# Kernel tuning notes

Measured on AMD Instinct MI355X. Metric: run time of the kernel, lower is better.

Reference implementation:

```python
import jax, jax.numpy as jnp
import numpy as np

B, L, D, H, DK, DV = 512, 256, 1024, 16, 64, 64
TEMP = float(np.sqrt(D))  # source uses sqrt(d_model), not sqrt(d_k)
LN_EPS = 1.0              # LayerNormalization default eps=1, added to std


def setup_inputs() -> dict:
    key = jax.random.key(0)
    ks = jax.random.split(key, 7)
    u = lambda k, shape: jax.random.uniform(k, shape, jnp.float32, -0.04, 0.04)
    return {
        "q": jax.random.normal(ks[0], (B, D), jnp.float32),
        "k": jax.random.normal(ks[1], (B, L, D), jnp.float32),
        "v": jax.random.normal(ks[2], (B, L, D), jnp.float32),
        "Wq": u(ks[3], (H, DK, D)),   # stacked per-head q-proj weights
        "Wk": u(ks[4], (H, DK, D)),
        "Wv": u(ks[5], (H, DV, D)),
        "Wp": u(ks[6], (D, H * DV)),  # output projection (nn.Linear weight layout)
        "scale": jnp.ones((D,), jnp.float32),
        "offset": jnp.zeros((D,), jnp.float32),
    }


def reference(q, k, v, Wq, Wk, Wv, Wp, scale, offset):
    # per-head projections (batched over heads instead of a Python loop)
    hq = jnp.einsum('bd,hkd->bhk', q, Wq)       # [B,H,DK]
    hk = jnp.einsum('bld,hkd->bhlk', k, Wk)     # [B,H,L,DK]
    hv = jnp.einsum('bld,hvd->bhlv', v, Wv)     # [B,H,L,DV]
    # single-query dot-product attention per head
    scores = jnp.einsum('bhk,bhlk->bhl', hq, hk) / TEMP
    w = jax.nn.softmax(scores, axis=-1)         # dropout is identity (rate 0 / eval)
    ctx = jnp.einsum('bhl,bhlv->bhv', w, hv).reshape(B, H * DV)
    # output projection + residual
    out = ctx @ Wp.T + q
    # LayerNormalization: unbiased std (torch.std default), eps added to std
    mean = out.mean(axis=-1, keepdims=True)
    std = jnp.sqrt(jnp.sum((out - mean) ** 2, axis=-1, keepdims=True) / (D - 1))
    return scale * (out - mean) / (std + LN_EPS) + offset
```

## Files before the change

### kernel.cpp

```cpp
#include <hip/hip_runtime.h>

#define B_ 512
#define L_ 256
#define D_ 1024
#define H_ 16
#define DK_ 64
#define DV_ 64

typedef float f32x4 __attribute__((ext_vector_type(4)));
typedef float f32x2 __attribute__((ext_vector_type(2)));
typedef __bf16 bf16x8 __attribute__((ext_vector_type(8)));
typedef __bf16 bf16x2 __attribute__((ext_vector_type(2)));

#define MFMA16(a, b, c) __builtin_amdgcn_mfma_f32_16x16x32_bf16((a), (b), (c), 0, 0, 0)

__device__ inline bf16x8 cvt8(f32x4 a, f32x4 b) {
  bf16x8 r;
  r[0] = (__bf16)a[0]; r[1] = (__bf16)a[1]; r[2] = (__bf16)a[2]; r[3] = (__bf16)a[3];
  r[4] = (__bf16)b[0]; r[5] = (__bf16)b[1]; r[6] = (__bf16)b[2]; r[7] = (__bf16)b[3];
  return r;
}

__global__ __launch_bounds__(256) void k_hq(const float* __restrict__ q,
                                            const float* __restrict__ Wq,
                                            __bf16* __restrict__ hq) {
  int tid = threadIdx.x, lane = tid & 63, wid = tid >> 6;
  int r16 = lane & 15, g = lane >> 4;
  int n0 = (blockIdx.x * 4 + wid) * 16;
  int m0 = blockIdx.y * 16;
  const float* arow = q  + (size_t)(m0 + r16) * D_;
  const float* brow = Wq + (size_t)(n0 + r16) * D_;
  f32x4 acc = {0.f, 0.f, 0.f, 0.f};
  for (int ks = 0; ks < D_ / 32; ++ks) {
    int k0 = ks * 32 + g * 8;
    f32x4 a0 = *(const f32x4*)(arow + k0);
    f32x4 a1 = *(const f32x4*)(arow + k0 + 4);
    f32x4 b0 = *(const f32x4*)(brow + k0);
    f32x4 b1 = *(const f32x4*)(brow + k0 + 4);
    acc = MFMA16(cvt8(a0, a1), cvt8(b0, b1), acc);
  }
#pragma unroll
  for (int r = 0; r < 4; ++r) {
    int m = m0 + g * 4 + r;
    hq[(size_t)m * (H_ * DK_) + n0 + r16] = (__bf16)acc[r];
  }
}

__global__ __launch_bounds__(256) void k_aq(const __bf16* __restrict__ hq,
                                            const float* __restrict__ Wk,
                                            __bf16* __restrict__ Aq) {
  int tid = threadIdx.x, lane = tid & 63, wid = tid >> 6;
  int r16 = lane & 15, g = lane >> 4;
  int h = blockIdx.z;
  int n0 = (blockIdx.x * 4 + wid) * 16;
  int m0 = blockIdx.y * 16;
  const __bf16* arow = hq + (size_t)(m0 + r16) * (H_ * DK_) + h * DK_;
  const float* bcol = Wk + (size_t)h * DK_ * D_ + n0 + r16;
  f32x4 acc = {0.f, 0.f, 0.f, 0.f};
#pragma unroll
  for (int ks = 0; ks < 2; ++ks) {
    int k0 = ks * 32 + g * 8;
    bf16x8 a = *(const bf16x8*)(arow + k0);
    f32x4 c0, c1;
#pragma unroll
    for (int j = 0; j < 4; ++j) c0[j] = bcol[(size_t)(k0 + j) * D_];
#pragma unroll
    for (int j = 0; j < 4; ++j) c1[j] = bcol[(size_t)(k0 + 4 + j) * D_];
    acc = MFMA16(a, cvt8(c0, c1), acc);
  }
#pragma unroll
  for (int r = 0; r < 4; ++r) {
    int m = m0 + g * 4 + r;
    Aq[(size_t)m * (H_ * D_) + (size_t)h * D_ + n0 + r16] = (__bf16)(acc[r] * 0.03125f);
  }
}

__global__ __launch_bounds__(256) void k_score(const float* __restrict__ kg,
                                               const __bf16* __restrict__ Aq,
                                               float* __restrict__ sc) {
  int tid = threadIdx.x, lane = tid & 63, wv = tid >> 6;
  int r16 = lane & 15, g = lane >> 4;
  int b = blockIdx.y;
  int l0 = blockIdx.x * 64 + wv * 16;
  const __bf16* AqB = Aq + (size_t)b * H_ * D_;
  const float*  kR  = kg + ((size_t)b * L_ + l0 + r16) * D_;
  f32x4 acc = {0.f, 0.f, 0.f, 0.f};
#pragma unroll 4
  for (int ks = 0; ks < D_ / 32; ++ks) {
    int k0 = ks * 32 + g * 8;
    bf16x8 a = *(const bf16x8*)(AqB + (size_t)r16 * D_ + k0);
    f32x4 b0 = *(const f32x4*)(kR + k0);
    f32x4 b1 = *(const f32x4*)(kR + k0 + 4);
    acc = MFMA16(a, cvt8(b0, b1), acc);
  }
#pragma unroll
  for (int r = 0; r < 4; ++r) {
    int h = g * 4 + r;
    sc[((size_t)b * H_ + h) * L_ + l0 + r16] = acc[r];
  }
}

__global__ __launch_bounds__(256) void k_cv(const float* __restrict__ vg,
                                            const float* __restrict__ sc,
                                            __bf16* __restrict__ cv) {
  __shared__ __bf16 wA[H_][L_ + 8];

  int tid = threadIdx.x, lane = tid & 63, wv = tid >> 6;
  int r16 = lane & 15, g = (lane >> 4) & 3;
  int b = blockIdx.y;

  const float* scB = sc + (size_t)b * H_ * L_;
#pragma unroll
  for (int rr = 0; rr < 4; ++rr) {
    int row = wv * 4 + rr;
    const float* srow = scB + (size_t)row * L_;
    float x0 = srow[lane], x1 = srow[lane + 64];
    float x2 = srow[lane + 128], x3 = srow[lane + 192];
    float m = fmaxf(fmaxf(x0, x1), fmaxf(x2, x3));
#pragma unroll
    for (int off = 32; off; off >>= 1) m = fmaxf(m, __shfl_xor(m, off));
    float e0 = __expf(x0 - m), e1 = __expf(x1 - m);
    float e2 = __expf(x2 - m), e3 = __expf(x3 - m);
    float s = e0 + e1 + e2 + e3;
#pragma unroll
    for (int off = 32; off; off >>= 1) s += __shfl_xor(s, off);
    float inv = 1.0f / s;
    wA[row][lane]       = (__bf16)(e0 * inv);
    wA[row][lane + 64]  = (__bf16)(e1 * inv);
    wA[row][lane + 128] = (__bf16)(e2 * inv);
    wA[row][lane + 192] = (__bf16)(e3 * inv);
  }
  __syncthreads();

  int dbase = blockIdx.x * 256 + wv * 64;
  const float* vB = vg + (size_t)b * L_ * D_ + dbase;
  f32x4 acc[4] = {{0.f,0.f,0.f,0.f},{0.f,0.f,0.f,0.f},
                  {0.f,0.f,0.f,0.f},{0.f,0.f,0.f,0.f}};
  for (int ks = 0; ks < 8; ++ks) {
    int l0 = ks * 32 + g * 8;
    bf16x8 a = *(const bf16x8*)(&wA[r16][l0]);
    const float* pv = vB + (size_t)l0 * D_ + r16;
#pragma unroll
    for (int nt = 0; nt < 4; ++nt) {
      const float* p = pv + nt * 16;
      f32x4 c0, c1;
#pragma unroll
      for (int j = 0; j < 4; ++j) c0[j] = p[(size_t)j * D_];
#pragma unroll
      for (int j = 0; j < 4; ++j) c1[j] = p[(size_t)(4 + j) * D_];
      acc[nt] = MFMA16(a, cvt8(c0, c1), acc[nt]);
    }
  }
#pragma unroll
  for (int nt = 0; nt < 4; ++nt)
#pragma unroll
    for (int r = 0; r < 4; ++r)
      cv[((size_t)b * H_ + g * 4 + r) * D_ + dbase + nt * 16 + r16] = (__bf16)acc[nt][r];
}

__global__ __launch_bounds__(256) void k_ctx(const __bf16* __restrict__ cv,
                                             const float* __restrict__ Wv,
                                             __bf16* __restrict__ ctx) {
  int tid = threadIdx.x, lane = tid & 63, wid = tid >> 6;
  int r16 = lane & 15, g = lane >> 4;
  int h = blockIdx.z, m0 = blockIdx.y * 16, n0 = wid * 16;
  const __bf16* arow = cv + (size_t)(m0 + r16) * (H_ * D_) + (size_t)h * D_;
  const float* brow = Wv + (size_t)h * DV_ * D_ + (size_t)(n0 + r16) * D_;
  f32x4 acc = {0.f, 0.f, 0.f, 0.f};
  for (int ks = 0; ks < D_ / 32; ++ks) {
    int k0 = ks * 32 + g * 8;
    bf16x8 a = *(const bf16x8*)(arow + k0);
    f32x4 b0 = *(const f32x4*)(brow + k0);
    f32x4 b1 = *(const f32x4*)(brow + k0 + 4);
    acc = MFMA16(a, cvt8(b0, b1), acc);
  }
#pragma unroll
  for (int r = 0; r < 4; ++r) {
    int m = m0 + g * 4 + r;
    ctx[(size_t)m * (H_ * DV_) + h * DV_ + n0 + r16] = (__bf16)acc[r];
  }
}

__global__ __launch_bounds__(256) void k_out(const __bf16* __restrict__ ctx,
                                             const float* __restrict__ Wp,
                                             const float* __restrict__ q,
                                             float* __restrict__ outp) {
  int tid = threadIdx.x, lane = tid & 63, wid = tid >> 6;
  int r16 = lane & 15, g = lane >> 4;
  int n0 = (blockIdx.x * 4 + wid) * 16;
  int m0 = blockIdx.y * 16;
  const __bf16* arow = ctx + (size_t)(m0 + r16) * D_;
  const float* brow = Wp + (size_t)(n0 + r16) * D_;
  f32x4 acc = {0.f, 0.f, 0.f, 0.f};
  for (int ks = 0; ks < D_ / 32; ++ks) {
    int k0 = ks * 32 + g * 8;
    bf16x8 a = *(const bf16x8*)(arow + k0);
    f32x4 b0 = *(const f32x4*)(brow + k0);
    f32x4 b1 = *(const f32x4*)(brow + k0 + 4);
    acc = MFMA16(a, cvt8(b0, b1), acc);
  }
#pragma unroll
  for (int r = 0; r < 4; ++r) {
    int m = m0 + g * 4 + r;
    outp[(size_t)m * D_ + n0 + r16] = acc[r] + q[(size_t)m * D_ + n0 + r16];
  }
}

__global__ __launch_bounds__(256) void k_ln(const float* __restrict__ xin,
                                            const float* __restrict__ scale,
                                            const float* __restrict__ offs,
                                            float* __restrict__ out) {
  __shared__ float red[4];
  int b = blockIdx.x, tid = threadIdx.x;
  const float* row = xin + (size_t)b * D_;
  f32x4 x = *(const f32x4*)(row + tid * 4);
  float s = x[0] + x[1] + x[2] + x[3];
#pragma unroll
  for (int off = 32; off; off >>= 1) s += __shfl_xor(s, off);
  if ((tid & 63) == 0) red[tid >> 6] = s;
  __syncthreads();
  float mean = (red[0] + red[1] + red[2] + red[3]) * (1.0f / D_);
  __syncthreads();
  float vs = 0.f;
#pragma unroll
  for (int j = 0; j < 4; ++j) { float d = x[j] - mean; vs += d * d; }
#pragma unroll
  for (int off = 32; off; off >>= 1) vs += __shfl_xor(vs, off);
  if ((tid & 63) == 0) red[tid >> 6] = vs;
  __syncthreads();
  float var = (red[0] + red[1] + red[2] + red[3]) * (1.0f / (D_ - 1));
  float inv = 1.0f / (sqrtf(var) + 1.0f);
  f32x4 sc = *(const f32x4*)(scale + tid * 4);
  f32x4 of = *(const f32x4*)(offs + tid * 4);
  f32x4 o;
#pragma unroll
  for (int j = 0; j < 4; ++j) o[j] = sc[j] * (x[j] - mean) * inv + of[j];
  *(f32x4*)(out + (size_t)b * D_ + tid * 4) = o;
}

extern "C" void kernel_launch(void* const* d_in, const int* in_sizes, int n_in,
                              void* d_out, int out_size, void* d_ws, size_t ws_size,
                              hipStream_t stream) {
  const float* q     = (const float*)d_in[0];
  const float* k     = (const float*)d_in[1];
  const float* v     = (const float*)d_in[2];
  const float* Wq    = (const float*)d_in[3];
  const float* Wk    = (const float*)d_in[4];
  const float* Wv    = (const float*)d_in[5];
  const float* Wp    = (const float*)d_in[6];
  const float* scale = (const float*)d_in[7];
  const float* offs  = (const float*)d_in[8];
  float* out = (float*)d_out;

  char* ws = (char*)d_ws;
  __bf16* hq   = (__bf16*)(ws);
  __bf16* Aq   = (__bf16*)(ws + (size_t)1  * (1 << 20));
  float*  scr  = (float*) (ws + (size_t)17 * (1 << 20));
  __bf16* cv   = (__bf16*)(ws + (size_t)25 * (1 << 20));
  __bf16* ctx  = (__bf16*)(ws + (size_t)41 * (1 << 20));
  float*  outp = (float*) (ws + (size_t)42 * (1 << 20));

  k_hq   <<<dim3(16, 32),     256, 0, stream>>>(q, Wq, hq);
  k_aq   <<<dim3(16, 32, 16), 256, 0, stream>>>(hq, Wk, Aq);
  k_score<<<dim3(4, 512),     256, 0, stream>>>(k, Aq, scr);
  k_cv   <<<dim3(4, 512),     256, 0, stream>>>(v, scr, cv);
  k_ctx  <<<dim3(1, 32, 16),  256, 0, stream>>>(cv, Wv, ctx);
  k_out  <<<dim3(16, 32),     256, 0, stream>>>(ctx, Wp, q, outp);
  k_ln   <<<dim3(512),        256, 0, stream>>>(outp, scale, offs, out);
}
```

Before: 312.9 us.

## Fuse q and key projection kernels and remap score/cv blocks across XCDs

Merges k_hq and k_aq into one kernel that computes the per-head query projection into LDS and immediately multiplies it by Wk. This removes the hq round trip through global memory and one launch. k_score and k_cv now use a 1D grid with a block-index swizzle that groups batches per XCD (stride-8 mapping), which should improve L2 locality for the shared Aq and score rows. It also adds an unroll-2 on the cv loop. The fused projection grid is smaller (512 blocks), which risks lower parallelism for the Wk stage.

```diff
diff --git a/kernel.cpp b/kernel.cpp
--- a/kernel.cpp
+++ b/kernel.cpp
@@ -21,57 +21,54 @@
   return r;
 }
 
-__global__ __launch_bounds__(256) void k_hq(const float* __restrict__ q,
-                                            const float* __restrict__ Wq,
-                                            __bf16* __restrict__ hq) {
+__global__ __launch_bounds__(256) void k_proj(const float* __restrict__ q,
+                                              const float* __restrict__ Wq,
+                                              const float* __restrict__ Wk,
+                                              __bf16* __restrict__ Aq) {
+  __shared__ __bf16 hq_lds[16][80];
   int tid = threadIdx.x, lane = tid & 63, wid = tid >> 6;
   int r16 = lane & 15, g = lane >> 4;
-  int n0 = (blockIdx.x * 4 + wid) * 16;
-  int m0 = blockIdx.y * 16;
-  const float* arow = q  + (size_t)(m0 + r16) * D_;
-  const float* brow = Wq + (size_t)(n0 + r16) * D_;
-  f32x4 acc = {0.f, 0.f, 0.f, 0.f};
-  for (int ks = 0; ks < D_ / 32; ++ks) {
-    int k0 = ks * 32 + g * 8;
-    f32x4 a0 = *(const f32x4*)(arow + k0);
-    f32x4 a1 = *(const f32x4*)(arow + k0 + 4);
-    f32x4 b0 = *(const f32x4*)(brow + k0);
-    f32x4 b1 = *(const f32x4*)(brow + k0 + 4);
-    acc = MFMA16(cvt8(a0, a1), cvt8(b0, b1), acc);
-  }
-#pragma unroll
-  for (int r = 0; r < 4; ++r) {
-    int m = m0 + g * 4 + r;
-    hq[(size_t)m * (H_ * DK_) + n0 + r16] = (__bf16)acc[r];
-  }
-}
-
-__global__ __launch_bounds__(256) void k_aq(const __bf16* __restrict__ hq,
-                                            const float* __restrict__ Wk,
-                                            __bf16* __restrict__ Aq) {
-  int tid = threadIdx.x, lane = tid & 63, wid = tid >> 6;
-  int r16 = lane & 15, g = lane >> 4;
-  int h = blockIdx.z;
-  int n0 = (blockIdx.x * 4 + wid) * 16;
-  int m0 = blockIdx.y * 16;
-  const __bf16* arow = hq + (size_t)(m0 + r16) * (H_ * DK_) + h * DK_;
-  const float* bcol = Wk + (size_t)h * DK_ * D_ + n0 + r16;
-  f32x4 acc = {0.f, 0.f, 0.f, 0.f};
-#pragma unroll
-  for (int ks = 0; ks < 2; ++ks) {
-    int k0 = ks * 32 + g * 8;
-    bf16x8 a = *(const bf16x8*)(arow + k0);
-    f32x4 c0, c1;
-#pragma unroll
-    for (int j = 0; j < 4; ++j) c0[j] = bcol[(size_t)(k0 + j) * D_];
-#pragma unroll
-    for (int j = 0; j < 4; ++j) c1[j] = bcol[(size_t)(k0 + 4 + j) * D_];
-    acc = MFMA16(a, cvt8(c0, c1), acc);
-  }
-#pragma unroll
-  for (int r = 0; r < 4; ++r) {
-    int m = m0 + g * 4 + r;
-    Aq[(size_t)m * (H_ * D_) + (size_t)h * D_ + n0 + r16] = (__bf16)(acc[r] * 0.03125f);
+  int m0 = blockIdx.x * 16, h = blockIdx.y;
+
+  {
+    const float* arow = q  + (size_t)(m0 + r16) * D_;
+    const float* brow = Wq + (size_t)(h * DK_ + wid * 16 + r16) * D_;
+    f32x4 acc = {0.f, 0.f, 0.f, 0.f};
+    for (int ks = 0; ks < D_ / 32; ++ks) {
+      int k0 = ks * 32 + g * 8;
+      f32x4 a0 = *(const f32x4*)(arow + k0);
+      f32x4 a1 = *(const f32x4*)(arow + k0 + 4);
+      f32x4 b0 = *(const f32x4*)(brow + k0);
+      f32x4 b1 = *(const f32x4*)(brow + k0 + 4);
+      acc = MFMA16(cvt8(a0, a1), cvt8(b0, b1), acc);
+    }
+#pragma unroll
+    for (int r = 0; r < 4; ++r)
+      hq_lds[g * 4 + r][wid * 16 + r16] = (__bf16)acc[r];
+  }
+  __syncthreads();
+
+  const float* bcolBase = Wk + (size_t)h * DK_ * D_;
+  for (int nt = 0; nt < 16; ++nt) {
+    int n0 = wid * 256 + nt * 16;
+    const float* bcol = bcolBase + n0 + r16;
+    f32x4 acc = {0.f, 0.f, 0.f, 0.f};
+#pragma unroll
+    for (int ks = 0; ks < 2; ++ks) {
+      int k0 = ks * 32 + g * 8;
+      bf16x8 a = *(const bf16x8*)(&hq_lds[r16][k0]);
+      f32x4 c0, c1;
+#pragma unroll
+      for (int j = 0; j < 4; ++j) c0[j] = bcol[(size_t)(k0 + j) * D_];
+#pragma unroll
+      for (int j = 0; j < 4; ++j) c1[j] = bcol[(size_t)(k0 + 4 + j) * D_];
+      acc = MFMA16(a, cvt8(c0, c1), acc);
+    }
+#pragma unroll
+    for (int r = 0; r < 4; ++r) {
+      int m = m0 + g * 4 + r;
+      Aq[(size_t)m * (H_ * D_) + (size_t)h * D_ + n0 + r16] = (__bf16)(acc[r] * 0.03125f);
+    }
   }
 }
 
@@ -80,8 +77,11 @@
                                                float* __restrict__ sc) {
   int tid = threadIdx.x, lane = tid & 63, wv = tid >> 6;
   int r16 = lane & 15, g = lane >> 4;
-  int b = blockIdx.y;
-  int l0 = blockIdx.x * 64 + wv * 16;
+  int wg = blockIdx.x;
+  int vid = (wg & 7) * 256 + (wg >> 3);
+  int b = vid >> 2;
+  int lq = vid & 3;
+  int l0 = lq * 64 + wv * 16;
   const __bf16* AqB = Aq + (size_t)b * H_ * D_;
   const float*  kR  = kg + ((size_t)b * L_ + l0 + r16) * D_;
   f32x4 acc = {0.f, 0.f, 0.f, 0.f};
@@ -107,7 +107,10 @@
 
   int tid = threadIdx.x, lane = tid & 63, wv = tid >> 6;
   int r16 = lane & 15, g = (lane >> 4) & 3;
-  int b = blockIdx.y;
+  int wg = blockIdx.x;
+  int vid = (wg & 7) * 256 + (wg >> 3);
+  int b = vid >> 2;
+  int dq = vid & 3;
 
   const float* scB = sc + (size_t)b * H_ * L_;
 #pragma unroll
@@ -132,10 +135,11 @@
   }
   __syncthreads();
 
-  int dbase = blockIdx.x * 256 + wv * 64;
+  int dbase = dq * 256 + wv * 64;
   const float* vB = vg + (size_t)b * L_ * D_ + dbase;
   f32x4 acc[4] = {{0.f,0.f,0.f,0.f},{0.f,0.f,0.f,0.f},
                   {0.f,0.f,0.f,0.f},{0.f,0.f,0.f,0.f}};
+#pragma unroll 2
   for (int ks = 0; ks < 8; ++ks) {
     int l0 = ks * 32 + g * 8;
     bf16x8 a = *(const bf16x8*)(&wA[r16][l0]);
@@ -253,17 +257,15 @@
   float* out = (float*)d_out;
 
   char* ws = (char*)d_ws;
-  __bf16* hq   = (__bf16*)(ws);
-  __bf16* Aq   = (__bf16*)(ws + (size_t)1  * (1 << 20));
-  float*  scr  = (float*) (ws + (size_t)17 * (1 << 20));
-  __bf16* cv   = (__bf16*)(ws + (size_t)25 * (1 << 20));
-  __bf16* ctx  = (__bf16*)(ws + (size_t)41 * (1 << 20));
-  float*  outp = (float*) (ws + (size_t)42 * (1 << 20));
-
-  k_hq   <<<dim3(16, 32),     256, 0, stream>>>(q, Wq, hq);
-  k_aq   <<<dim3(16, 32, 16), 256, 0, stream>>>(hq, Wk, Aq);
-  k_score<<<dim3(4, 512),     256, 0, stream>>>(k, Aq, scr);
-  k_cv   <<<dim3(4, 512),     256, 0, stream>>>(v, scr, cv);
+  __bf16* Aq   = (__bf16*)(ws);
+  float*  scr  = (float*) (ws + (size_t)16 * (1 << 20));
+  __bf16* cv   = (__bf16*)(ws + (size_t)24 * (1 << 20));
+  __bf16* ctx  = (__bf16*)(ws + (size_t)40 * (1 << 20));
+  float*  outp = (float*) (ws + (size_t)41 * (1 << 20));
+
+  k_proj <<<dim3(32, 16),     256, 0, stream>>>(q, Wq, Wk, Aq);
+  k_score<<<dim3(2048),       256, 0, stream>>>(k, Aq, scr);
+  k_cv   <<<dim3(2048),       256, 0, stream>>>(v, scr, cv);
   k_ctx  <<<dim3(1, 32, 16),  256, 0, stream>>>(cv, Wv, ctx);
   k_out  <<<dim3(16, 32),     256, 0, stream>>>(ctx, Wp, q, outp);
   k_ln   <<<dim3(512),        256, 0, stream>>>(outp, scale, offs, out);
```

Result: no change. 312.9 us (-0.0%).
